# Optimization experiments

Measured on AMD Instinct MI355X. Metric: run time of the kernel, lower is better.

## Reference

```python
import jax, jax.numpy as jnp
import numpy as np

NUM_HEADS = 16
EPS = 1e-5


def _layernorm(x, w):
    # torch LayerNorm (biased variance), bias=False
    m = jnp.mean(x, axis=-1, keepdims=True)
    v = jnp.mean(jnp.square(x - m), axis=-1, keepdims=True)
    return (x - m) * jax.lax.rsqrt(v + EPS) * w


def setup_inputs() -> dict:
    key = jax.random.key(0)
    ks = jax.random.split(key, 8)
    B, S, H, A = 2, 2048, 1024, 1024
    hd = H // NUM_HEADS
    return {
        "x": jax.random.normal(ks[0], (B, S, H), jnp.float32),
        "ada_cond": jax.random.normal(ks[1], (B, A), jnp.float32),
        "freqs": jax.random.normal(ks[2], (S, hd // 2, 2), jnp.float32),
        "w_qkv": jax.random.normal(ks[3], (3 * H, H), jnp.float32) * (1.0 / np.sqrt(H)),
        "w_o": jax.random.normal(ks[4], (H, H), jnp.float32) * (1.0 / np.sqrt(H)),
        "ln_w": jnp.ones((H,), jnp.float32),
        "mod_w": jax.random.normal(ks[5], (3 * H, A), jnp.float32) * 0.02,
        "mod_b": jax.random.normal(ks[6], (3 * H,), jnp.float32) * 0.02,
        "qn_w": jnp.ones((hd,), jnp.float32),
        "kn_w": jnp.ones((hd,), jnp.float32),
    }


def reference(x, ada_cond, freqs, w_qkv, w_o, ln_w, mod_w, mod_b, qn_w, kn_w):
    B, S, H = x.shape
    nh = NUM_HEADS
    hd = H // nh

    # pre-norm + AdaLN modulation (with gate)
    h = _layernorm(x, ln_w)
    mod = (jax.nn.silu(ada_cond) @ mod_w.T + mod_b)[:, None, :]  # [B,1,3H]
    scale, shift, gate = jnp.split(mod, 3, axis=-1)
    h = h * (scale + 1.0) + shift

    # QKV projection and head split
    qkv = h @ w_qkv.T                                  # [B,S,3H]
    q, k, v = jnp.split(qkv, 3, axis=-1)
    to_heads = lambda t: t.reshape(B, S, nh, hd).transpose(0, 2, 1, 3)  # [B,nh,S,hd]
    q, k, v = to_heads(q), to_heads(k), to_heads(v)

    # per-head QK layernorm
    q = _layernorm(q, qn_w)
    k = _layernorm(k, kn_w)

    # RoPE (complex rotation via interleaved pairs)
    f = freqs[:S].reshape(1, 1, S, hd // 2, 2)

    def rope(t):
        tr = t.reshape(B, nh, S, hd // 2, 2)
        re = tr[..., 0] * f[..., 0] - tr[..., 1] * f[..., 1]
        im = tr[..., 1] * f[..., 0] + tr[..., 0] * f[..., 1]
        return jnp.stack([re, im], axis=-1).reshape(B, nh, S, hd)

    q, k = rope(q), rope(k)

    # scaled dot-product attention (non-causal)
    scores = jnp.einsum("bhqd,bhkd->bhqk", q, k) * (1.0 / np.sqrt(hd))
    attn = jax.nn.softmax(scores, axis=-1)
    o = jnp.einsum("bhqk,bhkd->bhqd", attn, v)
    o = o.transpose(0, 2, 1, 3).reshape(B, S, H)

    return (o @ w_o.T) * gate
```

## Files before the change

kernel.cpp:

```cpp
#include <hip/hip_runtime.h>
#include <hip/hip_bf16.h>
#include <hip/hip_fp16.h>
#include <math.h>

#define B_ 2
#define S_ 2048
#define H_ 1024
#define A_ 1024
#define NH_ 16
#define HD_ 64
#define H3_ 3072
#define EPS_ 1e-5f

typedef __attribute__((ext_vector_type(8))) short short8;
typedef __attribute__((ext_vector_type(4))) float floatx4;
typedef __attribute__((ext_vector_type(4))) _Float16 half4v;
typedef __attribute__((ext_vector_type(2))) __fp16 fp16x2;

__device__ inline unsigned short f2bf(float x) {
    union { float f; unsigned u; } v; v.f = x;
    unsigned r = v.u + 0x7fffu + ((v.u >> 16) & 1u);
    return (unsigned short)(r >> 16);
}

__device__ inline unsigned pk_bf16(float a, float b) {
    union { __hip_bfloat162 h; unsigned u; } v;
    v.h = __float22bfloat162_rn(make_float2(a, b));
    return v.u;
}

__device__ inline unsigned pk_f16(float a, float b) {
    union { __half2 h; unsigned u; } v;
    v.h = __float22half2_rn(make_float2(a, b));
    return v.u;
}

__device__ inline void gld_lds16(const void* g, void* l) {
    __builtin_amdgcn_global_load_lds(
        (const __attribute__((address_space(1))) unsigned int*)g,
        (__attribute__((address_space(3))) unsigned int*)l, 16, 0, 0);
}

#define BARE_BARRIER() __builtin_amdgcn_s_barrier()


__global__ __launch_bounds__(256) void cast_bf16_kernel(
    const float* __restrict__ in, unsigned short* __restrict__ out, int n)
{
    int i = (blockIdx.x * 256 + threadIdx.x) * 8;
    if (i >= n) return;
    float4 a = *(const float4*)(in + i);
    float4 b = *(const float4*)(in + i + 4);
    uint4 o;
    o.x = pk_bf16(a.x, a.y);
    o.y = pk_bf16(a.z, a.w);
    o.z = pk_bf16(b.x, b.y);
    o.w = pk_bf16(b.z, b.w);
    *(uint4*)(out + i) = o;
}

__global__ __launch_bounds__(256) void mod_gemv_kernel(
    const float* __restrict__ ada, const float* __restrict__ mod_w,
    const float* __restrict__ mod_b, float* __restrict__ mod)
{
    int wid = threadIdx.x >> 6;
    int lane = threadIdx.x & 63;
    int idx = blockIdx.x * 4 + wid;
    int b = idx / H3_;
    int j = idx % H3_;
    const float* ar = ada + (size_t)b * A_;
    const float* wr = mod_w + (size_t)j * A_;
    float acc = 0.f;
    for (int a = lane; a < A_; a += 64) {
        float av = ar[a];
        float sv = av / (1.f + __expf(-av));
        acc += sv * wr[a];
    }
    #pragma unroll
    for (int m = 1; m < 64; m <<= 1) acc += __shfl_xor(acc, m);
    if (lane == 0) mod[idx] = acc + mod_b[j];
}

__global__ __launch_bounds__(256) void ln_mod_kernel(
    const float* __restrict__ x, const float* __restrict__ ln_w,
    const float* __restrict__ mod, unsigned short* __restrict__ hout)
{
    int row = blockIdx.x;
    int b = row >> 11;
    const float* xr = x + (size_t)row * H_;
    int t = threadIdx.x;
    float4 xv = *(const float4*)(xr + t * 4);
    float s1 = xv.x + xv.y + xv.z + xv.w;
    float s2 = xv.x*xv.x + xv.y*xv.y + xv.z*xv.z + xv.w*xv.w;
    #pragma unroll
    for (int m = 1; m < 64; m <<= 1) { s1 += __shfl_xor(s1, m); s2 += __shfl_xor(s2, m); }
    __shared__ float r1[4], r2[4];
    int wid = t >> 6, lane = t & 63;
    if (lane == 0) { r1[wid] = s1; r2[wid] = s2; }
    __syncthreads();
    s1 = r1[0] + r1[1] + r1[2] + r1[3];
    s2 = r2[0] + r2[1] + r2[2] + r2[3];
    float mean = s1 * (1.f / H_);
    float var  = s2 * (1.f / H_) - mean * mean;
    float rstd = rsqrtf(var + EPS_);
    const float* mrow = mod + (size_t)b * H3_;
    float4 wv = *(const float4*)(ln_w + t * 4);
    float4 sc = *(const float4*)(mrow + t * 4);
    float4 sh = *(const float4*)(mrow + H_ + t * 4);
    float4 hv;
    hv.x = (xv.x - mean) * rstd * wv.x * (sc.x + 1.f) + sh.x;
    hv.y = (xv.y - mean) * rstd * wv.y * (sc.y + 1.f) + sh.y;
    hv.z = (xv.z - mean) * rstd * wv.z * (sc.z + 1.f) + sh.z;
    hv.w = (xv.w - mean) * rstd * wv.w * (sc.w + 1.f) + sh.w;
    uint2 o;
    o.x = pk_bf16(hv.x, hv.y);
    o.y = pk_bf16(hv.z, hv.w);
    *(uint2*)(hout + (size_t)row * H_ + t * 4) = o;
}

__global__ __launch_bounds__(256) void gemm_qkv_fused_kernel(
    const unsigned short* __restrict__ A, const unsigned short* __restrict__ Bm,
    const float* __restrict__ freqs, const float* __restrict__ qn_w,
    const float* __restrict__ kn_w, unsigned short* __restrict__ qout,
    unsigned short* __restrict__ kout, unsigned short* __restrict__ vtout)
{
    __shared__ unsigned short As[2][128 * 64];
    __shared__ unsigned short Bs[2][128 * 64];
    const int K = H_;
    const int NIT = K / 64;
    int t = threadIdx.x;
    int w = t >> 6, lane = t & 63;
    int q16 = lane & 15, quad = lane >> 4;
    int wm = w >> 1, wn = w & 1;
    int m0 = blockIdx.y * 128, n0 = blockIdx.x * 128;

    int srow = lane >> 3;
    int scol = ((lane & 7) ^ ((lane >> 3) & 7)) << 3;
    const unsigned short* ga = A + (size_t)(m0 + (w << 5) + srow) * K + scol;
    const unsigned short* gb = Bm + (size_t)(n0 + (w << 5) + srow) * K + scol;

    floatx4 acc[4][4];
    #pragma unroll
    for (int mt = 0; mt < 4; ++mt)
        #pragma unroll
        for (int nt = 0; nt < 4; ++nt)
            acc[mt][nt] = (floatx4){0.f, 0.f, 0.f, 0.f};

    int arow = (wm * 64 + q16) * 64;
    int brow = (wn * 64 + q16) * 64;
    int sw0 = ((quad ^ (q16 & 7)) << 3);
    int sw1 = (((4 + quad) ^ (q16 & 7)) << 3);

    #pragma unroll
    for (int p = 0; p < 2; ++p) {
        #pragma unroll
        for (int j = 0; j < 4; ++j) {
            gld_lds16(ga + p * 64 + (size_t)(j * 8) * K, &As[p][(w * 32 + j * 8) * 64]);
            gld_lds16(gb + p * 64 + (size_t)(j * 8) * K, &Bs[p][(w * 32 + j * 8) * 64]);
        }
    }

    for (int kt = 0; kt < NIT; ++kt) {
        int cb = kt & 1;
        if (kt < NIT - 1) asm volatile("s_waitcnt vmcnt(8)" ::: "memory");
        else              asm volatile("s_waitcnt vmcnt(0)" ::: "memory");
        BARE_BARRIER();

        const unsigned short* curA = &As[cb][0];
        const unsigned short* curB = &Bs[cb][0];

        __builtin_amdgcn_s_setprio(1);
        #pragma unroll
        for (int ks = 0; ks < 2; ++ks) {
            int sw = ks ? sw1 : sw0;
            short8 af[4], bf[4];
            #pragma unroll
            for (int mt = 0; mt < 4; ++mt)
                af[mt] = *(const short8*)&curA[arow + mt * 1024 + sw];
            #pragma unroll
            for (int nt = 0; nt < 4; ++nt)
                bf[nt] = *(const short8*)&curB[brow + nt * 1024 + sw];
            #pragma unroll
            for (int mt = 0; mt < 4; ++mt)
                #pragma unroll
                for (int nt = 0; nt < 4; ++nt)
                    acc[mt][nt] = __builtin_amdgcn_mfma_f32_16x16x32_bf16(
                        af[mt], bf[nt], acc[mt][nt], 0, 0, 0);
        }
        __builtin_amdgcn_s_setprio(0);

        asm volatile("s_waitcnt lgkmcnt(0)" ::: "memory");
        BARE_BARRIER();

        if (kt + 2 < NIT) {
            const unsigned short* ga2 = ga + (kt + 2) * 64;
            const unsigned short* gb2 = gb + (kt + 2) * 64;
            #pragma unroll
            for (int j = 0; j < 4; ++j) {
                gld_lds16(ga2 + (size_t)(j * 8) * K, &As[cb][(w * 32 + j * 8) * 64]);
                gld_lds16(gb2 + (size_t)(j * 8) * K, &Bs[cb][(w * 32 + j * 8) * 64]);
            }
        }
    }

    int n_base = n0 + wn * 64;
    int sec = n_base >> 10;
    int head = (n_base & 1023) >> 6;

    if (sec == 2) {
        #pragma unroll
        for (int mt = 0; mt < 4; ++mt) {
            int m = m0 + wm * 64 + mt * 16 + quad * 4;
            int b = m >> 11, s = m & (S_ - 1);
            #pragma unroll
            for (int nt = 0; nt < 4; ++nt) {
                int d = nt * 16 + q16;
                unsigned short* dst =
                    vtout + ((size_t)((b * 16 + head) * 64 + d)) * S_ + s;
                uint2 pk;
                pk.x = pk_f16(acc[mt][nt][0], acc[mt][nt][1]);
                pk.y = pk_f16(acc[mt][nt][2], acc[mt][nt][3]);
                *(uint2*)dst = pk;
            }
        }
    } else {
        const float* nw = (sec == 0) ? qn_w : kn_w;
        float w4[4];
        #pragma unroll
        for (int nt = 0; nt < 4; ++nt) w4[nt] = nw[nt * 16 + q16];
        unsigned short* outp = (sec == 0) ? qout : kout;
        float qscale = (sec == 0) ? 0.1803368801111244f : 1.0f;

        #pragma unroll
        for (int mt = 0; mt < 4; ++mt) {
            #pragma unroll
            for (int i = 0; i < 4; ++i) {
                int m = m0 + wm * 64 + mt * 16 + quad * 4 + i;
                int b = m >> 11, s = m & (S_ - 1);
                float v0 = acc[mt][0][i], v1 = acc[mt][1][i];
                float v2 = acc[mt][2][i], v3 = acc[mt][3][i];
                float s1 = (v0 + v1) + (v2 + v3);
                float s2 = (v0 * v0 + v1 * v1) + (v2 * v2 + v3 * v3);
                #pragma unroll
                for (int msk = 1; msk < 16; msk <<= 1) {
                    s1 += __shfl_xor(s1, msk);
                    s2 += __shfl_xor(s2, msk);
                }
                float mean = s1 * (1.f / 64);
                float var  = s2 * (1.f / 64) - mean * mean;
                float rstd = rsqrtf(var + EPS_);
                float vv[4];
                vv[0] = (v0 - mean) * rstd * w4[0];
                vv[1] = (v1 - mean) * rstd * w4[1];
                vv[2] = (v2 - mean) * rstd * w4[2];
                vv[3] = (v3 - mean) * rstd * w4[3];
                const float* fr = freqs + (size_t)s * 64;
                unsigned short* orow = outp + ((size_t)((b * 16 + head) * S_ + s)) * 64;
                #pragma unroll
                for (int nt = 0; nt < 4; ++nt) {
                    int c = nt * 16 + q16;
                    float vp = __shfl_xor(vv[nt], 1);
                    float2 ff = *(const float2*)(fr + (c & ~1));
                    float r = (c & 1) ? (vv[nt] * ff.x + vp * ff.y)
                                      : (vv[nt] * ff.x - vp * ff.y);
                    orow[c] = f2bf(r * qscale);
                }
            }
        }
    }
}

__global__ __launch_bounds__(256) void gemm_bt_bf16_kernel(
    const unsigned short* __restrict__ A, const unsigned short* __restrict__ Bm,
    float* __restrict__ C, int M, int N, int K,
    const float* __restrict__ gate, int gate_stride, int batch_shift)
{
    __shared__ unsigned short As[2][128 * 64];
    __shared__ unsigned short Bs[2][64 * 64];
    const int NIT = 1024 / 64;
    int t = threadIdx.x;
    int w = t >> 6, lane = t & 63;
    int q16 = lane & 15, quad = lane >> 4;
    int m0 = blockIdx.y * 128, n0 = blockIdx.x * 64;

    int srow = lane >> 3;
    int scol = ((lane & 7) ^ ((lane >> 3) & 7)) << 3;
    const unsigned short* ga = A + (size_t)(m0 + (w << 5) + srow) * K + scol;
    const unsigned short* gb = Bm + (size_t)(n0 + (w << 4) + srow) * K + scol;

    floatx4 acc[2][4];
    #pragma unroll
    for (int mt = 0; mt < 2; ++mt)
        #pragma unroll
        for (int nt = 0; nt < 4; ++nt)
            acc[mt][nt] = (floatx4){0.f, 0.f, 0.f, 0.f};

    int arow = (w * 32 + q16) * 64;
    int brow = q16 * 64;
    int sw0 = ((quad ^ (q16 & 7)) << 3);
    int sw1 = (((4 + quad) ^ (q16 & 7)) << 3);

    #pragma unroll
    for (int p = 0; p < 2; ++p) {
        #pragma unroll
        for (int j = 0; j < 4; ++j)
            gld_lds16(ga + p * 64 + (size_t)(j * 8) * K, &As[p][(w * 32 + j * 8) * 64]);
        #pragma unroll
        for (int j = 0; j < 2; ++j)
            gld_lds16(gb + p * 64 + (size_t)(j * 8) * K, &Bs[p][(w * 16 + j * 8) * 64]);
    }

    for (int kt = 0; kt < NIT; ++kt) {
        int cb = kt & 1;
        if (kt < NIT - 1) asm volatile("s_waitcnt vmcnt(6)" ::: "memory");
        else              asm volatile("s_waitcnt vmcnt(0)" ::: "memory");
        BARE_BARRIER();

        const unsigned short* curA = &As[cb][0];
        const unsigned short* curB = &Bs[cb][0];

        __builtin_amdgcn_s_setprio(1);
        #pragma unroll
        for (int ks = 0; ks < 2; ++ks) {
            int sw = ks ? sw1 : sw0;
            short8 af[2], bf[4];
            #pragma unroll
            for (int mt = 0; mt < 2; ++mt)
                af[mt] = *(const short8*)&curA[arow + mt * 1024 + sw];
            #pragma unroll
            for (int nt = 0; nt < 4; ++nt)
                bf[nt] = *(const short8*)&curB[brow + nt * 1024 + sw];
            #pragma unroll
            for (int mt = 0; mt < 2; ++mt)
                #pragma unroll
                for (int nt = 0; nt < 4; ++nt)
                    acc[mt][nt] = __builtin_amdgcn_mfma_f32_16x16x32_bf16(
                        af[mt], bf[nt], acc[mt][nt], 0, 0, 0);
        }
        __builtin_amdgcn_s_setprio(0);

        asm volatile("s_waitcnt lgkmcnt(0)" ::: "memory");
        BARE_BARRIER();

        if (kt + 2 < NIT) {
            const unsigned short* ga2 = ga + (kt + 2) * 64;
            const unsigned short* gb2 = gb + (kt + 2) * 64;
            #pragma unroll
            for (int j = 0; j < 4; ++j)
                gld_lds16(ga2 + (size_t)(j * 8) * K, &As[cb][(w * 32 + j * 8) * 64]);
            #pragma unroll
            for (int j = 0; j < 2; ++j)
                gld_lds16(gb2 + (size_t)(j * 8) * K, &Bs[cb][(w * 16 + j * 8) * 64]);
        }
    }

    #pragma unroll
    for (int mt = 0; mt < 2; ++mt) {
        #pragma unroll
        for (int i = 0; i < 4; ++i) {
            int m = m0 + w * 32 + mt * 16 + quad * 4 + i;
            float* crow = C + (size_t)m * N;
            const float* grow = gate ? gate + (size_t)(m >> batch_shift) * gate_stride
                                     : nullptr;
            #pragma unroll
            for (int nt = 0; nt < 4; ++nt) {
                int n = n0 + nt * 16 + q16;
                float v = acc[mt][nt][i];
                if (gate) v *= grow[n];
                crow[n] = v;
            }
        }
    }
}

__global__ __launch_bounds__(256, 2) void attn_mfma_kernel(
    const unsigned short* __restrict__ q, const unsigned short* __restrict__ k,
    const unsigned short* __restrict__ vt, unsigned short* __restrict__ o)
{
    __shared__ __align__(16) unsigned char smem[16 * 1024];
    __shared__ float lbuf[4][4][16];
    unsigned short* Vs = (unsigned short*)smem;

    int t = threadIdx.x;
    int w = t >> 6, lane = t & 63;
    int q16 = lane & 15, quad = lane >> 4;
    int bh = blockIdx.y, b = bh >> 4, h = bh & 15;
    int s0 = blockIdx.x * 64;

    const unsigned short* qgp = q + ((size_t)bh * S_ + s0) * HD_;
    short8 qf[4][2];
    #pragma unroll
    for (int qg = 0; qg < 4; ++qg)
        #pragma unroll
        for (int hh = 0; hh < 2; ++hh)
            qf[qg][hh] = *(const short8*)(qgp + (16 * qg + q16) * HD_ + hh * 32 + quad * 8);

    const unsigned short* kg = k + (size_t)bh * S_ * HD_ + (16 * w + q16) * HD_ + quad * 8;

    const unsigned short* vg0 = vt + (size_t)bh * 64 * S_
                              + (size_t)(16 * w + (lane >> 3)) * S_ + (lane & 7) * 8;
    const unsigned short* vg1 = vg0 + 8 * S_;
    unsigned short* vw0 = Vs + (16 * w + (lane >> 3)) * 64 + (((lane & 7) ^ (lane >> 3)) << 3);
    unsigned short* vw1 = vw0 + 512;
    int vroff = q16 * 64 + (((2 * w + (quad >> 1)) ^ (q16 & 7)) << 3) + ((quad & 1) << 2);

    const int NT = S_ / 64;

    short8 kf_nx0 = *(const short8*)kg;
    short8 kf_nx1 = *(const short8*)(kg + 32);
    uint4 vr0 = *(const uint4*)vg0;
    uint4 vr1 = *(const uint4*)vg1;
    vg0 += 64; vg1 += 64;

    *(uint4*)vw0 = vr0;
    *(uint4*)vw1 = vr1;
    vr0 = *(const uint4*)vg0;
    vr1 = *(const uint4*)vg1;
    vg0 += 64; vg1 += 64;
    asm volatile("s_waitcnt lgkmcnt(0)" ::: "memory");
    BARE_BARRIER();

    union { half4v h; uint2 u; } ones;
    ones.u.x = 0x3C003C00u; ones.u.y = 0x3C003C00u;

    floatx4 acc_o[4][4];
    floatx4 acc_l[4];
    #pragma unroll
    for (int nd = 0; nd < 4; ++nd)
        #pragma unroll
        for (int qg = 0; qg < 4; ++qg)
            acc_o[nd][qg] = (floatx4){0.f, 0.f, 0.f, 0.f};
    #pragma unroll
    for (int qg = 0; qg < 4; ++qg) acc_l[qg] = (floatx4){0.f, 0.f, 0.f, 0.f};

    int cur = 0;
    for (int kt = 0; kt < NT; ++kt) {
        short8 kf0 = kf_nx0, kf1 = kf_nx1;

        if (kt + 1 < NT) {
            int nb = cur ^ 1;
            *(uint4*)(vw0 + nb * 4096) = vr0;
            *(uint4*)(vw1 + nb * 4096) = vr1;
            kg += 64 * HD_;
            kf_nx0 = *(const short8*)kg;
            kf_nx1 = *(const short8*)(kg + 32);
            if (kt + 2 < NT) {
                vr0 = *(const uint4*)vg0;
                vr1 = *(const uint4*)vg1;
                vg0 += 64; vg1 += 64;
            }
        }

        floatx4 sc[4];
        #pragma unroll
        for (int qg = 0; qg < 4; ++qg) sc[qg] = (floatx4){-12.f, -12.f, -12.f, -12.f};
        __builtin_amdgcn_s_setprio(1);
        #pragma unroll
        for (int qg = 0; qg < 4; ++qg) {
            sc[qg] = __builtin_amdgcn_mfma_f32_16x16x32_bf16(kf0, qf[qg][0], sc[qg], 0, 0, 0);
            sc[qg] = __builtin_amdgcn_mfma_f32_16x16x32_bf16(kf1, qf[qg][1], sc[qg], 0, 0, 0);
        }

        const unsigned short* vbase = Vs + cur * 4096;
        half4v vf[4];
        #pragma unroll
        for (int nd = 0; nd < 4; ++nd)
            vf[nd] = *(const half4v*)&vbase[vroff + nd * 1024];

        #pragma unroll
        for (int qg = 0; qg < 4; ++qg) {
            float p0 = __builtin_amdgcn_exp2f(sc[qg][0]);
            float p1 = __builtin_amdgcn_exp2f(sc[qg][1]);
            float p2 = __builtin_amdgcn_exp2f(sc[qg][2]);
            float p3 = __builtin_amdgcn_exp2f(sc[qg][3]);
            union { half4v h; fp16x2 f2[2]; } pf;
            pf.f2[0] = __builtin_amdgcn_cvt_pkrtz(p0, p1);
            pf.f2[1] = __builtin_amdgcn_cvt_pkrtz(p2, p3);
            acc_l[qg] = __builtin_amdgcn_mfma_f32_16x16x16f16(ones.h, pf.h, acc_l[qg], 0, 0, 0);
            #pragma unroll
            for (int nd = 0; nd < 4; ++nd)
                acc_o[nd][qg] = __builtin_amdgcn_mfma_f32_16x16x16f16(
                    vf[nd], pf.h, acc_o[nd][qg], 0, 0, 0);
        }
        __builtin_amdgcn_s_setprio(0);

        asm volatile("s_waitcnt lgkmcnt(0)" ::: "memory");
        BARE_BARRIER();
        cur ^= 1;
    }

    if (quad == 0) {
        #pragma unroll
        for (int qg = 0; qg < 4; ++qg) lbuf[w][qg][q16] = acc_l[qg][0];
    }
    __syncthreads();
    float linv = 1.f / (lbuf[0][w][q16] + lbuf[1][w][q16] + lbuf[2][w][q16] + lbuf[3][w][q16]);

    float* obuf = (float*)smem;
    float* myw = obuf + ((w * 4) * 64 + lane) * 4;
    float* myr = obuf + (w * 64 + lane) * 4;
    unsigned short* og = o + ((size_t)(b * S_ + s0 + 16 * w + q16)) * H_ + h * HD_ + 4 * quad;

    #pragma unroll
    for (int nd = 0; nd < 4; ++nd) {
        __syncthreads();
        #pragma unroll
        for (int qg = 0; qg < 4; ++qg)
            *(floatx4*)(myw + qg * 256) = acc_o[nd][qg];
        __syncthreads();
        floatx4 r0 = *(const floatx4*)(myr);
        floatx4 r1 = *(const floatx4*)(myr + 1024);
        floatx4 r2 = *(const floatx4*)(myr + 2048);
        floatx4 r3 = *(const floatx4*)(myr + 3072);
        floatx4 s = (r0 + r1) + (r2 + r3);
        uint2 pk;
        pk.x = pk_bf16(s[0] * linv, s[1] * linv);
        pk.y = pk_bf16(s[2] * linv, s[3] * linv);
        *(uint2*)(og + nd * 16) = pk;
    }
}

extern "C" void kernel_launch(void* const* d_in, const int* in_sizes, int n_in,
                              void* d_out, int out_size, void* d_ws, size_t ws_size,
                              hipStream_t stream)
{
    const float* x     = (const float*)d_in[0];
    const float* ada   = (const float*)d_in[1];
    const float* freqs = (const float*)d_in[2];
    const float* w_qkv = (const float*)d_in[3];
    const float* w_o   = (const float*)d_in[4];
    const float* ln_w  = (const float*)d_in[5];
    const float* mod_w = (const float*)d_in[6];
    const float* mod_b = (const float*)d_in[7];
    const float* qn_w  = (const float*)d_in[8];
    const float* kn_w  = (const float*)d_in[9];
    float* out = (float*)d_out;

    float* ws  = (float*)d_ws;
    float* mod = ws;
    unsigned short* hb    = (unsigned short*)(mod + 8192);
    unsigned short* qb    = hb + (size_t)B_ * S_ * H_;
    unsigned short* kb    = qb + (size_t)B_ * S_ * H_;
    unsigned short* vtb   = kb + (size_t)B_ * S_ * H_;
    unsigned short* ob    = vtb + (size_t)B_ * S_ * H_;
    unsigned short* wqkvb = ob + (size_t)B_ * S_ * H_;
    unsigned short* wob   = wqkvb + (size_t)H3_ * H_;

    cast_bf16_kernel<<<H3_ * H_ / (8 * 256), 256, 0, stream>>>(w_qkv, wqkvb, H3_ * H_);
    cast_bf16_kernel<<<H_ * H_ / (8 * 256), 256, 0, stream>>>(w_o, wob, H_ * H_);
    mod_gemv_kernel<<<B_ * H3_ / 4, 256, 0, stream>>>(ada, mod_w, mod_b, mod);
    ln_mod_kernel<<<B_ * S_, 256, 0, stream>>>(x, ln_w, mod, hb);
    gemm_qkv_fused_kernel<<<dim3(H3_ / 128, B_ * S_ / 128), 256, 0, stream>>>(
        hb, wqkvb, freqs, qn_w, kn_w, qb, kb, vtb);
    attn_mfma_kernel<<<dim3(S_ / 64, B_ * NH_), 256, 0, stream>>>(qb, kb, vtb, ob);
    gemm_bt_bf16_kernel<<<dim3(H_ / 64, B_ * S_ / 128), 256, 0, stream>>>(
        ob, wob, out, B_ * S_, H_, H_, mod + 2 * H_, H3_, 11);
}
```

Baseline: 235.3 us.

## Process two key tiles per iteration using 16x16x32 f16 MFMA for PV

```diff
diff --git a/kernel.cpp b/kernel.cpp
--- a/kernel.cpp
+++ b/kernel.cpp
@@ -15,6 +15,7 @@
 typedef __attribute__((ext_vector_type(8))) short short8;
 typedef __attribute__((ext_vector_type(4))) float floatx4;
 typedef __attribute__((ext_vector_type(4))) _Float16 half4v;
+typedef __attribute__((ext_vector_type(8))) _Float16 half8v;
 typedef __attribute__((ext_vector_type(2))) __fp16 fp16x2;
 
 __device__ inline unsigned short f2bf(float x) {
@@ -42,7 +43,6 @@
 }
 
 #define BARE_BARRIER() __builtin_amdgcn_s_barrier()
-
 
 __global__ __launch_bounds__(256) void cast_bf16_kernel(
     const float* __restrict__ in, unsigned short* __restrict__ out, int n)
@@ -377,7 +377,7 @@
     const unsigned short* __restrict__ q, const unsigned short* __restrict__ k,
     const unsigned short* __restrict__ vt, unsigned short* __restrict__ o)
 {
-    __shared__ __align__(16) unsigned char smem[16 * 1024];
+    __shared__ __align__(16) unsigned char smem[32 * 1024];
     __shared__ float lbuf[4][4][16];
     unsigned short* Vs = (unsigned short*)smem;
 
@@ -400,28 +400,37 @@
     const unsigned short* vg0 = vt + (size_t)bh * 64 * S_
                               + (size_t)(16 * w + (lane >> 3)) * S_ + (lane & 7) * 8;
     const unsigned short* vg1 = vg0 + 8 * S_;
-    unsigned short* vw0 = Vs + (16 * w + (lane >> 3)) * 64 + (((lane & 7) ^ (lane >> 3)) << 3);
-    unsigned short* vw1 = vw0 + 512;
+    int vwoff0 = (16 * w + (lane >> 3)) * 64 + (((lane & 7) ^ (lane >> 3)) << 3);
+    int vwoff1 = vwoff0 + 512;
     int vroff = q16 * 64 + (((2 * w + (quad >> 1)) ^ (q16 & 7)) << 3) + ((quad & 1) << 2);
 
-    const int NT = S_ / 64;
-
-    short8 kf_nx0 = *(const short8*)kg;
-    short8 kf_nx1 = *(const short8*)(kg + 32);
-    uint4 vr0 = *(const uint4*)vg0;
-    uint4 vr1 = *(const uint4*)vg1;
-    vg0 += 64; vg1 += 64;
-
-    *(uint4*)vw0 = vr0;
-    *(uint4*)vw1 = vr1;
-    vr0 = *(const uint4*)vg0;
-    vr1 = *(const uint4*)vg1;
-    vg0 += 64; vg1 += 64;
+    const int NP = S_ / 128;
+
+    short8 kfa0n = *(const short8*)kg;
+    short8 kfa1n = *(const short8*)(kg + 32);
+    short8 kfb0n = *(const short8*)(kg + 4096);
+    short8 kfb1n = *(const short8*)(kg + 4096 + 32);
+    uint4 vra0 = *(const uint4*)vg0;
+    uint4 vra1 = *(const uint4*)vg1;
+    uint4 vrb0 = *(const uint4*)(vg0 + 64);
+    uint4 vrb1 = *(const uint4*)(vg1 + 64);
+    vg0 += 128; vg1 += 128;
+
+    *(uint4*)(Vs + vwoff0) = vra0;
+    *(uint4*)(Vs + vwoff1) = vra1;
+    *(uint4*)(Vs + 4096 + vwoff0) = vrb0;
+    *(uint4*)(Vs + 4096 + vwoff1) = vrb1;
+    vra0 = *(const uint4*)vg0;
+    vra1 = *(const uint4*)vg1;
+    vrb0 = *(const uint4*)(vg0 + 64);
+    vrb1 = *(const uint4*)(vg1 + 64);
+    vg0 += 128; vg1 += 128;
     asm volatile("s_waitcnt lgkmcnt(0)" ::: "memory");
     BARE_BARRIER();
 
-    union { half4v h; uint2 u; } ones;
-    ones.u.x = 0x3C003C00u; ones.u.y = 0x3C003C00u;
+    union { half8v h; unsigned u[4]; } ones;
+    ones.u[0] = 0x3C003C00u; ones.u[1] = 0x3C003C00u;
+    ones.u[2] = 0x3C003C00u; ones.u[3] = 0x3C003C00u;
 
     floatx4 acc_o[4][4];
     floatx4 acc_l[4];
@@ -433,60 +442,82 @@
     #pragma unroll
     for (int qg = 0; qg < 4; ++qg) acc_l[qg] = (floatx4){0.f, 0.f, 0.f, 0.f};
 
-    int cur = 0;
-    for (int kt = 0; kt < NT; ++kt) {
-        short8 kf0 = kf_nx0, kf1 = kf_nx1;
-
-        if (kt + 1 < NT) {
-            int nb = cur ^ 1;
-            *(uint4*)(vw0 + nb * 4096) = vr0;
-            *(uint4*)(vw1 + nb * 4096) = vr1;
-            kg += 64 * HD_;
-            kf_nx0 = *(const short8*)kg;
-            kf_nx1 = *(const short8*)(kg + 32);
-            if (kt + 2 < NT) {
-                vr0 = *(const uint4*)vg0;
-                vr1 = *(const uint4*)vg1;
-                vg0 += 64; vg1 += 64;
+    for (int i = 0; i < NP; ++i) {
+        int cur = i & 1;
+        short8 kfa0 = kfa0n, kfa1 = kfa1n;
+        short8 kfb0 = kfb0n, kfb1 = kfb1n;
+
+        if (i + 1 < NP) {
+            unsigned short* wb = Vs + (cur ^ 1) * 8192;
+            *(uint4*)(wb + vwoff0) = vra0;
+            *(uint4*)(wb + vwoff1) = vra1;
+            *(uint4*)(wb + 4096 + vwoff0) = vrb0;
+            *(uint4*)(wb + 4096 + vwoff1) = vrb1;
+            kg += 128 * HD_;
+            kfa0n = *(const short8*)kg;
+            kfa1n = *(const short8*)(kg + 32);
+            kfb0n = *(const short8*)(kg + 4096);
+            kfb1n = *(const short8*)(kg + 4096 + 32);
+            if (i + 2 < NP) {
+                vra0 = *(const uint4*)vg0;
+                vra1 = *(const uint4*)vg1;
+                vrb0 = *(const uint4*)(vg0 + 64);
+                vrb1 = *(const uint4*)(vg1 + 64);
+                vg0 += 128; vg1 += 128;
             }
         }
 
-        floatx4 sc[4];
-        #pragma unroll
-        for (int qg = 0; qg < 4; ++qg) sc[qg] = (floatx4){-12.f, -12.f, -12.f, -12.f};
+        floatx4 sa[4], sb[4];
+        #pragma unroll
+        for (int qg = 0; qg < 4; ++qg) {
+            sa[qg] = (floatx4){-12.f, -12.f, -12.f, -12.f};
+            sb[qg] = (floatx4){-12.f, -12.f, -12.f, -12.f};
+        }
         __builtin_amdgcn_s_setprio(1);
         #pragma unroll
         for (int qg = 0; qg < 4; ++qg) {
-            sc[qg] = __builtin_amdgcn_mfma_f32_16x16x32_bf16(kf0, qf[qg][0], sc[qg], 0, 0, 0);
-            sc[qg] = __builtin_amdgcn_mfma_f32_16x16x32_bf16(kf1, qf[qg][1], sc[qg], 0, 0, 0);
-        }
-
-        const unsigned short* vbase = Vs + cur * 4096;
-        half4v vf[4];
-        #pragma unroll
-        for (int nd = 0; nd < 4; ++nd)
-            vf[nd] = *(const half4v*)&vbase[vroff + nd * 1024];
+            sa[qg] = __builtin_amdgcn_mfma_f32_16x16x32_bf16(kfa0, qf[qg][0], sa[qg], 0, 0, 0);
+            sa[qg] = __builtin_amdgcn_mfma_f32_16x16x32_bf16(kfa1, qf[qg][1], sa[qg], 0, 0, 0);
+            sb[qg] = __builtin_amdgcn_mfma_f32_16x16x32_bf16(kfb0, qf[qg][0], sb[qg], 0, 0, 0);
+            sb[qg] = __builtin_amdgcn_mfma_f32_16x16x32_bf16(kfb1, qf[qg][1], sb[qg], 0, 0, 0);
+        }
+
+        const unsigned short* va = Vs + cur * 8192;
+        const unsigned short* vb = va + 4096;
+        half8v vf[4];
+        #pragma unroll
+        for (int nd = 0; nd < 4; ++nd) {
+            union { half8v v8; half4v v4[2]; } u;
+            u.v4[0] = *(const half4v*)&va[vroff + nd * 1024];
+            u.v4[1] = *(const half4v*)&vb[vroff + nd * 1024];
+            vf[nd] = u.v8;
+        }
 
         #pragma unroll
         for (int qg = 0; qg < 4; ++qg) {
-            float p0 = __builtin_amdgcn_exp2f(sc[qg][0]);
-            float p1 = __builtin_amdgcn_exp2f(sc[qg][1]);
-            float p2 = __builtin_amdgcn_exp2f(sc[qg][2]);
-            float p3 = __builtin_amdgcn_exp2f(sc[qg][3]);
-            union { half4v h; fp16x2 f2[2]; } pf;
-            pf.f2[0] = __builtin_amdgcn_cvt_pkrtz(p0, p1);
-            pf.f2[1] = __builtin_amdgcn_cvt_pkrtz(p2, p3);
-            acc_l[qg] = __builtin_amdgcn_mfma_f32_16x16x16f16(ones.h, pf.h, acc_l[qg], 0, 0, 0);
+            float a0 = __builtin_amdgcn_exp2f(sa[qg][0]);
+            float a1 = __builtin_amdgcn_exp2f(sa[qg][1]);
+            float a2 = __builtin_amdgcn_exp2f(sa[qg][2]);
+            float a3 = __builtin_amdgcn_exp2f(sa[qg][3]);
+            float b0 = __builtin_amdgcn_exp2f(sb[qg][0]);
+            float b1 = __builtin_amdgcn_exp2f(sb[qg][1]);
+            float b2 = __builtin_amdgcn_exp2f(sb[qg][2]);
+            float b3 = __builtin_amdgcn_exp2f(sb[qg][3]);
+            union { half8v h; fp16x2 f2[4]; } pf;
+            pf.f2[0] = __builtin_amdgcn_cvt_pkrtz(a0, a1);
+            pf.f2[1] = __builtin_amdgcn_cvt_pkrtz(a2, a3);
+            pf.f2[2] = __builtin_amdgcn_cvt_pkrtz(b0, b1);
+            pf.f2[3] = __builtin_amdgcn_cvt_pkrtz(b2, b3);
+            acc_l[qg] = __builtin_amdgcn_mfma_f32_16x16x32_f16(ones.h, pf.h, acc_l[qg], 0, 0, 0);
             #pragma unroll
             for (int nd = 0; nd < 4; ++nd)
-                acc_o[nd][qg] = __builtin_amdgcn_mfma_f32_16x16x16f16(
+                acc_o[nd][qg] = __builtin_amdgcn_mfma_f32_16x16x32_f16(
                     vf[nd], pf.h, acc_o[nd][qg], 0, 0, 0);
         }
         __builtin_amdgcn_s_setprio(0);
 
         asm volatile("s_waitcnt lgkmcnt(0)" ::: "memory");
         BARE_BARRIER();
-        cur ^= 1;
     }
 
     if (quad == 0) {
```

Measured after the change: 230.4 us. 2.1% less time.
